# Optimization experiments

Measured on AMD Instinct MI355X. Metric: run time of the kernel, lower is better.

Reference implementation:

```python
import jax, jax.numpy as jnp
import numpy as np

N, E, DIN, HID, H, ED = 50000, 800000, 128, 64, 4, 5
Z_IDX = 3          # impedance column
PHYS_W = 1.0       # physics_weight
NEG_SLOPE = 0.2    # GATv2 leaky_relu slope


def gat_layer(x, src, dst, ea, Wl, bl, Wr, br, We, att, temp, bias, concat):
    """PhysicsGATv2Conv (add_self_loops=False, eval mode / no dropout)."""
    n = x.shape[0]
    Hh, C = att.shape
    xl = (x @ Wl + bl).reshape(n, Hh, C)   # lin_l -> source features
    xr = (x @ Wr + br).reshape(n, Hh, C)   # lin_r -> target features
    # physics-enhanced edge attr: overwrite last column with temp * w / |Z|
    z = jnp.clip(ea[:, Z_IDX], 1e-6, None)
    ea = ea.at[:, -1].set(temp * PHYS_W / z)
    e = (ea @ We).reshape(-1, Hh, C)       # lin_edge (no bias)
    m = jax.nn.leaky_relu(xl[src] + xr[dst] + e, NEG_SLOPE)  # [E,H,C]
    logit = jnp.einsum('ehc,hc->eh', m, att)                 # [E,H]
    # segment softmax over incoming edges of each target node
    lmax = jax.ops.segment_max(logit, dst, num_segments=n)
    w = jnp.exp(logit - lmax[dst])
    den = jax.ops.segment_sum(w, dst, num_segments=n)
    a = w / (den[dst] + 1e-16)
    out = jax.ops.segment_sum(xl[src] * a[:, :, None], dst, num_segments=n)
    out = out.reshape(n, Hh * C) if concat else out.mean(axis=1)
    return out + bias


def layer_norm(x, w, b):
    mu = x.mean(-1, keepdims=True)
    v = ((x - mu) ** 2).mean(-1, keepdims=True)
    return (x - mu) * jax.lax.rsqrt(v + 1e-5) * w + b


def setup_inputs() -> dict:
    key = jax.random.key(0)
    ks = iter(jax.random.split(key, 40))
    nk = lambda: next(ks)
    d = {}
    d['x'] = jax.random.normal(nk(), (N, DIN), jnp.float32)
    d['edge_index'] = jax.random.randint(nk(), (2, E), 0, N)
    d['edge_attr'] = jax.random.uniform(nk(), (E, ED), jnp.float32)
    hd = HID * H
    cfg = [(DIN, True), (hd, True), (hd, False)]
    for i, (din, concat) in enumerate(cfg):
        dout = hd if concat else HID
        d[f'Wl{i}'] = jax.random.normal(nk(), (din, hd), jnp.float32) / np.sqrt(din)
        d[f'bl{i}'] = 0.01 * jax.random.normal(nk(), (hd,), jnp.float32)
        d[f'Wr{i}'] = jax.random.normal(nk(), (din, hd), jnp.float32) / np.sqrt(din)
        d[f'br{i}'] = 0.01 * jax.random.normal(nk(), (hd,), jnp.float32)
        d[f'We{i}'] = jax.random.normal(nk(), (ED, hd), jnp.float32) / np.sqrt(ED)
        d[f'att{i}'] = jax.random.normal(nk(), (H, HID), jnp.float32) / np.sqrt(HID)
        d[f'temp{i}'] = jnp.float32(1.0)
        d[f'bias{i}'] = 0.01 * jax.random.normal(nk(), (dout,), jnp.float32)
        d[f'lnw{i}'] = jnp.ones((dout,), jnp.float32)
        d[f'lnb{i}'] = jnp.zeros((dout,), jnp.float32)
    d['pw0'] = jax.random.normal(nk(), (DIN, hd), jnp.float32) / np.sqrt(DIN)
    d['pb0'] = jnp.zeros((hd,), jnp.float32)
    d['pw2'] = jax.random.normal(nk(), (hd, HID), jnp.float32) / np.sqrt(hd)
    d['pb2'] = jnp.zeros((HID,), jnp.float32)
    return d


def reference(x, edge_index, edge_attr,
              Wl0, bl0, Wr0, br0, We0, att0, temp0, bias0, lnw0, lnb0,
              Wl1, bl1, Wr1, br1, We1, att1, temp1, bias1, lnw1, lnb1,
              Wl2, bl2, Wr2, br2, We2, att2, temp2, bias2, lnw2, lnb2,
              pw0, pb0, pw2, pb2):
    src, dst = edge_index[0], edge_index[1]
    # layer 0: 128 -> 256 (concat), residual projected
    h = gat_layer(x, src, dst, edge_attr, Wl0, bl0, Wr0, br0, We0, att0, temp0, bias0, True)
    h = layer_norm(h, lnw0, lnb0) + (x @ pw0 + pb0)
    h = jax.nn.elu(h)
    # layer 1: 256 -> 256 (concat), identity residual
    h1 = gat_layer(h, src, dst, edge_attr, Wl1, bl1, Wr1, br1, We1, att1, temp1, bias1, True)
    h = layer_norm(h1, lnw1, lnb1) + h
    h = jax.nn.elu(h)
    # layer 2: 256 -> 64 (head-mean), residual projected, no activation
    h2 = gat_layer(h, src, dst, edge_attr, Wl2, bl2, Wr2, br2, We2, att2, temp2, bias2, False)
    out = layer_norm(h2, lnw2, lnb2) + (h @ pw2 + pb2)
    return out
```

## Files before the change

kernel.cpp:

```cpp
#include <hip/hip_runtime.h>
#include <math.h>

#define NN 50000
#define EE 800000
#define NB 196

typedef _Float16 half8 __attribute__((ext_vector_type(8)));
typedef _Float16 hv4  __attribute__((ext_vector_type(4)));
typedef _Float16 hv2  __attribute__((ext_vector_type(2)));
typedef __fp16 fp16v2 __attribute__((ext_vector_type(2)));
typedef float floatx16 __attribute__((ext_vector_type(16)));
typedef float fv4 __attribute__((ext_vector_type(4)));

__device__ __forceinline__ float fexp2(float x) { return __builtin_amdgcn_exp2f(x); }

template<int CTRL>
__device__ __forceinline__ float dppadd(float x) {
    int t = __builtin_amdgcn_update_dpp(0, __float_as_int(x), CTRL, 0xf, 0xf, false);
    return x + __int_as_float(t);
}
__device__ __forceinline__ float red16(float x) {
    x = dppadd<0x121>(x);
    x = dppadd<0x122>(x);
    x = dppadd<0x124>(x);
    x = dppadd<0x128>(x);
    return x;
}

__device__ __forceinline__ unsigned int dup16(float x) {
    unsigned short b = __builtin_bit_cast(unsigned short, (_Float16)x);
    return (unsigned int)b * 0x10001u;
}
__device__ __forceinline__ unsigned int duph(float x) {
#if __has_builtin(__builtin_amdgcn_cvt_pkrtz)
    fp16v2 p = __builtin_amdgcn_cvt_pkrtz(x, x);
    return __builtin_bit_cast(unsigned int, p);
#else
    return dup16(x);
#endif
}
__device__ __forceinline__ hv4 b4(unsigned int u) {
    hv2 p = __builtin_bit_cast(hv2, u);
    return (hv4){p[0], p[1], p[0], p[1]};
}
__device__ __forceinline__ float dot4h(hv4 a, hv4 b, float c) {
    hv2 al = {a[0], a[1]}, ah = {a[2], a[3]};
    hv2 bl = {b[0], b[1]}, bh = {b[2], b[3]};
#if __has_builtin(__builtin_amdgcn_fdot2)
    return __builtin_amdgcn_fdot2(al, bl, __builtin_amdgcn_fdot2(ah, bh, c, false), false);
#else
    return c + (float)a[0]*(float)b[0] + (float)a[1]*(float)b[1]
             + (float)a[2]*(float)b[2] + (float)a[3]*(float)b[3];
#endif
}

__global__ __launch_bounds__(256) void swizzleA(
    const float* __restrict__ A, _Float16* __restrict__ Asw, int M, int K)
{
    int wave = threadIdx.x >> 6, lane = threadIdx.x & 63;
    int tile = blockIdx.x;
    int kc = blockIdx.y * 4 + wave;
    int KC = K >> 4;
    if (kc >= KC) return;
    int row = tile * 32 + (lane & 31);
    int k0 = kc * 16 + (lane >> 5) * 8;
    float4 v0 = make_float4(0.f, 0.f, 0.f, 0.f);
    float4 v1 = make_float4(0.f, 0.f, 0.f, 0.f);
    if (row < M) {
        const float* p = A + (size_t)row * K + k0;
        v0 = *(const float4*)p;
        v1 = *(const float4*)(p + 4);
    }
    half8 o;
    o[0] = (_Float16)v0.x; o[1] = (_Float16)v0.y;
    o[2] = (_Float16)v0.z; o[3] = (_Float16)v0.w;
    o[4] = (_Float16)v1.x; o[5] = (_Float16)v1.y;
    o[6] = (_Float16)v1.z; o[7] = (_Float16)v1.w;
    *(half8*)(Asw + (((size_t)tile * KC + kc) * 64 + lane) * 8) = o;
}

__global__ __launch_bounds__(256) void prep_weights(
    const float* __restrict__ s0, const float* __restrict__ s1,
    const float* __restrict__ s2, const float* __restrict__ s3,
    const float* __restrict__ s4, const float* __restrict__ s5,
    const float* __restrict__ s6, const float* __restrict__ s7,
    _Float16* __restrict__ catB0, _Float16* __restrict__ catB1,
    _Float16* __restrict__ catB2,
    const float* __restrict__ bl0, const float* __restrict__ br0,
    const float* __restrict__ pb0, const float* __restrict__ bl1,
    const float* __restrict__ br1, const float* __restrict__ bl2,
    const float* __restrict__ br2, const float* __restrict__ pb2,
    float* __restrict__ cb0, float* __restrict__ cb1, float* __restrict__ cb2,
    const float* __restrict__ We0a, const float* __restrict__ We1a,
    const float* __restrict__ We2a, const float* __restrict__ att0a,
    const float* __restrict__ att1a, const float* __restrict__ att2a,
    _Float16* __restrict__ Weh)
{
    int b = blockIdx.x;
    if (b == 192) {
        const float* Ws[3] = {We0a, We1a, We2a};
        const float* As[3] = {att0a, att1a, att2a};
        for (int t = threadIdx.x; t < 4608; t += 256) {
            int l = t / 1536, o = t - l * 1536;
            float v = (o < 1280) ? Ws[l][o] : As[l][o - 1280];
            Weh[t] = (_Float16)v;
        }
        return;
    }
    if (b >= 184) {
        int t = (b - 184) * 256 + threadIdx.x;
        if (t < 768) {
            cb0[t] = (t < 256) ? bl0[t] : (t < 512) ? br0[t - 256] : pb0[t - 512];
        } else if (t < 1280) {
            int u = t - 768;
            cb1[u] = (u < 256) ? bl1[u] : br1[u - 256];
        } else if (t < 1856) {
            int u = t - 1280;
            cb2[u] = (u < 256) ? bl2[u] : (u < 512) ? br2[u - 256] : pb2[u - 512];
        }
        return;
    }
    int wave = threadIdx.x >> 6, lane = threadIdx.x & 63;
    int pair = b * 4 + wave;
    const int cum[9] = {0, 64, 128, 192, 320, 448, 576, 704, 736};
    int job = 0;
    while (pair >= cum[job + 1]) ++job;
    const float* srcs[8] = {s0, s1, s2, s3, s4, s5, s6, s7};
    const int KCs[8] = {8, 8, 8, 16, 16, 16, 16, 16};
    const int NCs[8] = {256, 256, 256, 256, 256, 256, 256, 64};
    const int ntb[8] = {0, 8, 16, 0, 8, 0, 8, 16};
    _Float16* dsts[8] = {catB0, catB0, catB0, catB1, catB1, catB2, catB2, catB2};
    int p = pair - cum[job];
    int KC = KCs[job], NC = NCs[job];
    int nt = p / KC, kc = p - nt * KC;
    int n = (nt >> 1) * 64 + ((lane & 31) * 2) + (nt & 1);
    int k0 = kc * 16 + (lane >> 5) * 8;
    const float* B = srcs[job];
    half8 o;
#pragma unroll
    for (int jj = 0; jj < 8; ++jj)
        o[jj] = (_Float16)B[(size_t)(k0 + jj) * NC + n];
    int ntG = ntb[job] + nt;
    *(half8*)(dsts[job] + (((size_t)ntG * KC + kc) * 64 + lane) * 8) = o;
}

__global__ __launch_bounds__(256) void gemm_mfma(
    const _Float16* __restrict__ Asw, const _Float16* __restrict__ Bsw,
    const float* __restrict__ bias, _Float16* __restrict__ C,
    int M, int K, int NC)
{
    const int wave = threadIdx.x >> 6, lane = threadIdx.x & 63;
    const int KC = K >> 4;
    const int rt0 = blockIdx.x * 4 + (wave & 1) * 2;
    const int NG = NC >> 6;
    int g = blockIdx.y * 2 + (wave >> 1);
    if (g >= NG) g = NG - 1;

    const half8* Ap0 = (const half8*)Asw + (size_t)rt0 * KC * 64 + lane;
    const half8* Ap1 = Ap0 + (size_t)KC * 64;
    const half8* Bp0 = (const half8*)Bsw + (size_t)(2 * g) * KC * 64 + lane;
    const half8* Bp1 = Bp0 + (size_t)KC * 64;

    floatx16 accE0 = {0.f}, accE1 = {0.f}, accO0 = {0.f}, accO1 = {0.f};

#pragma unroll 4
    for (int kc = 0; kc < KC; ++kc) {
        half8 a0 = Ap0[(size_t)kc * 64];
        half8 a1 = Ap1[(size_t)kc * 64];
        half8 b0 = Bp0[(size_t)kc * 64];
        half8 b1 = Bp1[(size_t)kc * 64];
        accE0 = __builtin_amdgcn_mfma_f32_32x32x16_f16(a0, b0, accE0, 0, 0, 0);
        accE1 = __builtin_amdgcn_mfma_f32_32x32x16_f16(a1, b0, accE1, 0, 0, 0);
        accO0 = __builtin_amdgcn_mfma_f32_32x32x16_f16(a0, b1, accO0, 0, 0, 0);
        accO1 = __builtin_amdgcn_mfma_f32_32x32x16_f16(a1, b1, accO1, 0, 0, 0);
    }

    const int nlane = lane & 31, hs = lane >> 5;
    int colb = g * 64 + nlane * 2;
    float be = bias[colb], bo = bias[colb + 1];
#pragma unroll
    for (int r = 0; r < 16; ++r) {
        int rowin = (r & 3) + 8 * (r >> 2) + 4 * hs;
        int row0 = rt0 * 32 + rowin;
        int row1 = row0 + 32;
        if (row0 < M) {
            hv2 pe;
            pe[0] = (_Float16)(accE0[r] + be);
            pe[1] = (_Float16)(accO0[r] + bo);
            *(hv2*)(C + (size_t)row0 * NC + colb) = pe;
        }
        if (row1 < M) {
            hv2 po;
            po[0] = (_Float16)(accE1[r] + be);
            po[1] = (_Float16)(accO1[r] + bo);
            *(hv2*)(C + (size_t)row1 * NC + colb) = po;
        }
    }
}

__global__ __launch_bounds__(256) void hist_kernel(const int* __restrict__ dst,
                                                   int* __restrict__ deg)
{
    int e = blockIdx.x * 256 + threadIdx.x;
    if (e < EE) atomicAdd(&deg[dst[e]], 1);
}

__global__ __launch_bounds__(256) void scan_local(const int* __restrict__ deg,
                                                  int* __restrict__ rowoff,
                                                  int* __restrict__ part)
{
    __shared__ int sd[256];
    int tid = threadIdx.x;
    int i = blockIdx.x * 256 + tid;
    int v = (i < NN) ? deg[i] : 0;
    sd[tid] = v;
    __syncthreads();
    for (int off = 1; off < 256; off <<= 1) {
        int t = (tid >= off) ? sd[tid - off] : 0;
        __syncthreads();
        sd[tid] += t;
        __syncthreads();
    }
    if (i < NN) rowoff[i] = sd[tid] - v;
    if (tid == 255) part[blockIdx.x] = sd[255];
}

__global__ __launch_bounds__(256) void scan_part(int* __restrict__ part,
                                                 int* __restrict__ rowoff)
{
    __shared__ int sd[256];
    int tid = threadIdx.x;
    int v = (tid < NB) ? part[tid] : 0;
    sd[tid] = v;
    __syncthreads();
    for (int off = 1; off < 256; off <<= 1) {
        int t = (tid >= off) ? sd[tid - off] : 0;
        __syncthreads();
        sd[tid] += t;
        __syncthreads();
    }
    if (tid < NB) part[tid] = sd[tid] - v;
    if (tid == 0) rowoff[NN] = EE;
}

__global__ __launch_bounds__(256) void scan_add(int* __restrict__ rowoff,
                                                const int* __restrict__ part,
                                                int* __restrict__ cursor)
{
    int i = blockIdx.x * 256 + threadIdx.x;
    if (i < NN) {
        rowoff[i] += part[blockIdx.x];
        cursor[i] = 0;
    }
}

__global__ __launch_bounds__(256) void scatter_kernel(
    const int* __restrict__ src, const int* __restrict__ dst,
    const float* __restrict__ ea, const int* __restrict__ rowoff,
    int* __restrict__ cursor, int* __restrict__ srcp,
    unsigned int* __restrict__ apk, float* __restrict__ erec)
{
    int e = blockIdx.x * 256 + threadIdx.x;
    if (e < EE) {
        int d = dst[e];
        int pos = rowoff[d] + atomicAdd(&cursor[d], 1);
        srcp[pos] = src[e];
        const float* p = ea + (size_t)e * 5;
        uint4 o;
        o.x = dup16(p[0]); o.y = dup16(p[1]);
        o.z = dup16(p[2]); o.w = dup16(p[3]);
        *(uint4*)(apk + (size_t)pos * 4) = o;
        erec[pos] = 1.0f / fmaxf(p[3], 1e-6f);
    }
}

__global__ __launch_bounds__(256) void build_qtab(
    const float* __restrict__ erec, const float* __restrict__ temp,
    unsigned int* __restrict__ qtab)
{
    int e = blockIdx.x * 256 + threadIdx.x;
    if (e >= EE) return;
    float q = temp[0] * erec[e];
    float qs = fminf(q, 64.f);
    float inv = (q > 64.f) ? 64.f * __builtin_amdgcn_rcpf(q) : 1.0f;
    float sl = fmaxf(q * 0.015625f, 1.f) * 1.44269504088896340736f;
    uint4 o;
    o.x = dup16(qs);
    o.y = dup16(inv);
    o.z = __builtin_bit_cast(unsigned int, sl);
    o.w = 0u;
    *(uint4*)(qtab + (size_t)e * 4) = o;
}

template<int MODE, int RSTRIDE>
__global__ __launch_bounds__(256) void fused_attn_ln(
    const int* __restrict__ rowoff, const int* __restrict__ srcp,
    const unsigned int* __restrict__ apk, const unsigned int* __restrict__ qtab,
    const _Float16* __restrict__ xlp, const _Float16* __restrict__ Wh,
    const float* __restrict__ bias, const float* __restrict__ lnw,
    const float* __restrict__ lnb,
    const _Float16* __restrict__ residH, const float* __restrict__ residF,
    float* __restrict__ outF, _Float16* __restrict__ aswOut)
{
    int v = __builtin_amdgcn_readfirstlane(blockIdx.x * 4 + (threadIdx.x >> 6));
    int lane = threadIdx.x & 63;
    if (v >= NN) return;
    int grp = lane >> 4;
    int sub = lane & 15;
    int j = grp * 64 + sub * 4;

    hv4 ww0h = *(const hv4*)(Wh + j);
    hv4 ww1h = *(const hv4*)(Wh + 256 + j);
    hv4 ww2h = *(const hv4*)(Wh + 512 + j);
    hv4 ww3h = *(const hv4*)(Wh + 768 + j);
    hv4 ww4h = *(const hv4*)(Wh + 1024 + j);
    hv4 atvh = *(const hv4*)(Wh + 1280 + j);
    hv4 xrvh = *(const hv4*)(xlp + (size_t)v * RSTRIDE + 256 + j);
    const _Float16 s02 = (_Float16)0.2f;
    const hv4 sl02 = {s02, s02, s02, s02};
    const float L2E = 1.44269504088896340736f;

    float mxd = -INFINITY, dend = 0.f;
    fv4 acc = {0.f, 0.f, 0.f, 0.f};

    int beg = __builtin_amdgcn_readfirstlane(rowoff[v]);
    int end = __builtin_amdgcn_readfirstlane(rowoff[v + 1]);
    int i = beg;
    for (; i + 4 <= end; i += 4) {
        int s[4]; uint4 ap[4], qt[4]; hv4 xh[4]; float l[4];
#pragma unroll
        for (int u = 0; u < 4; ++u) {
            s[u] = __builtin_amdgcn_readfirstlane(srcp[i + u]);
            ap[u] = *(const uint4*)(apk + (size_t)(i + u) * 4);
            qt[u] = *(const uint4*)(qtab + (size_t)(i + u) * 4);
        }
#pragma unroll
        for (int u = 0; u < 4; ++u)
            xh[u] = *(const hv4*)(xlp + (size_t)s[u] * RSTRIDE + j);
#pragma unroll
        for (int u = 0; u < 4; ++u) {
            hv4 t = xh[u] + xrvh;
            t += b4(ap[u].x) * ww0h;
            t += b4(ap[u].y) * ww1h;
            t += b4(ap[u].z) * ww2h;
            t += b4(ap[u].w) * ww3h;
            hv4 m = b4(qt[u].x) * ww4h;
            m += b4(qt[u].y) * t;
            hv4 mn = m * sl02;
            m = __builtin_elementwise_max(m, mn);
            l[u] = dot4h(m, atvh, 0.f);
        }
#pragma unroll
        for (int u = 0; u < 4; ++u)
            l[u] = red16(l[u]) * __builtin_bit_cast(float, qt[u].z);
        float nm = fmaxf(fmaxf(l[0], l[1]), fmaxf(l[2], l[3]));
        nm = fmaxf(nm, mxd);
        float sc = fexp2(mxd - nm);
        float e0 = fexp2(l[0] - nm);
        float e1 = fexp2(l[1] - nm);
        float e2 = fexp2(l[2] - nm);
        float e3 = fexp2(l[3] - nm);
        mxd = nm;
        dend = dend * sc + ((e0 + e1) + (e2 + e3));
        hv4 X = xh[0] * b4(duph(e0));
        X += xh[1] * b4(duph(e1));
        X += xh[2] * b4(duph(e2));
        X += xh[3] * b4(duph(e3));
        fv4 Xf = __builtin_convertvector(X, fv4);
        acc = acc * sc + Xf;
    }
    for (; i < end; ++i) {
        int s0 = __builtin_amdgcn_readfirstlane(srcp[i]);
        uint4 ap = *(const uint4*)(apk + (size_t)i * 4);
        uint4 qt = *(const uint4*)(qtab + (size_t)i * 4);
        hv4 xh = *(const hv4*)(xlp + (size_t)s0 * RSTRIDE + j);
        hv4 t = xh + xrvh;
        t += b4(ap.x) * ww0h;
        t += b4(ap.y) * ww1h;
        t += b4(ap.z) * ww2h;
        t += b4(ap.w) * ww3h;
        hv4 m = b4(qt.x) * ww4h;
        m += b4(qt.y) * t;
        hv4 mn = m * sl02;
        m = __builtin_elementwise_max(m, mn);
        float l0 = dot4h(m, atvh, 0.f);
        l0 = red16(l0) * __builtin_bit_cast(float, qt.z);
        float nm = fmaxf(mxd, l0);
        float sc = fexp2(mxd - nm);
        float e0 = fexp2(l0 - nm);
        mxd = nm;
        dend = dend * sc + e0;
        fv4 xf = __builtin_convertvector(xh, fv4);
        acc = acc * sc + xf * e0;
    }

    float inv = __builtin_amdgcn_rcpf(dend + 1e-16f);
    if (MODE <= 1) {
        fv4 bb = *(const fv4*)(bias + j);
        fv4 o = acc * inv + bb;
        float s  = (o[0] + o[1]) + (o[2] + o[3]);
        fv4 oq = o * o;
        float s2 = (oq[0] + oq[1]) + (oq[2] + oq[3]);
        s = red16(s);   s += __shfl_xor(s, 16, 64);  s += __shfl_xor(s, 32, 64);
        s2 = red16(s2); s2 += __shfl_xor(s2, 16, 64); s2 += __shfl_xor(s2, 32, 64);
        float mu = s * (1.f / 256.f);
        float var = s2 * (1.f / 256.f) - mu * mu;
        float rs = __builtin_amdgcn_rsqf(var + 1e-5f);
        fv4 lw = *(const fv4*)(lnw + j);
        fv4 lb = *(const fv4*)(lnb + j);
        fv4 rr;
        if (MODE == 0)
            rr = __builtin_convertvector(
                *(const hv4*)(residH + (size_t)v * RSTRIDE + j), fv4);
        else
            rr = *(const fv4*)(residF + (size_t)v * 256 + j);
        fv4 y = (o - mu) * rs * lw + lb + rr;
        y[0] = (y[0] > 0.f) ? y[0] : fexp2(y[0] * L2E) - 1.f;
        y[1] = (y[1] > 0.f) ? y[1] : fexp2(y[1] * L2E) - 1.f;
        y[2] = (y[2] > 0.f) ? y[2] : fexp2(y[2] * L2E) - 1.f;
        y[3] = (y[3] > 0.f) ? y[3] : fexp2(y[3] * L2E) - 1.f;
        if (MODE == 0)
            *(fv4*)(outF + (size_t)v * 256 + j) = y;
        int kc = j >> 4, half = (j >> 3) & 1, off = j & 7;
        size_t idx = (((size_t)(v >> 5) * 16 + kc) * 64 + (v & 31) + 32 * half) * 8 + off;
        hv4 yh = __builtin_convertvector(y, hv4);
        *(hv4*)(aswOut + idx) = yh;
    } else {
        fv4 r = acc * inv;
        r[0] += __shfl_xor(r[0], 16, 64); r[0] += __shfl_xor(r[0], 32, 64);
        r[1] += __shfl_xor(r[1], 16, 64); r[1] += __shfl_xor(r[1], 32, 64);
        r[2] += __shfl_xor(r[2], 16, 64); r[2] += __shfl_xor(r[2], 32, 64);
        r[3] += __shfl_xor(r[3], 16, 64); r[3] += __shfl_xor(r[3], 32, 64);
        fv4 bb = *(const fv4*)(bias + sub * 4);
        fv4 o = r * 0.25f + bb;
        float s  = (o[0] + o[1]) + (o[2] + o[3]);
        fv4 oq = o * o;
        float s2 = (oq[0] + oq[1]) + (oq[2] + oq[3]);
        s = red16(s);
        s2 = red16(s2);
        float mu = s * (1.f / 64.f);
        float var = s2 * (1.f / 64.f) - mu * mu;
        float rs = __builtin_amdgcn_rsqf(var + 1e-5f);
        fv4 lw = *(const fv4*)(lnw + sub * 4);
        fv4 lb = *(const fv4*)(lnb + sub * 4);
        fv4 rr = __builtin_convertvector(
            *(const hv4*)(residH + (size_t)v * RSTRIDE + sub * 4), fv4);
        fv4 y = (o - mu) * rs * lw + lb + rr;
        if (grp == 0)
            *(fv4*)(outF + (size_t)v * 64 + sub * 4) = y;
    }
}

extern "C" void kernel_launch(void* const* d_in, const int* in_sizes, int n_in,
                              void* d_out, int out_size, void* d_ws, size_t ws_size,
                              hipStream_t stream)
{
    const float* x    = (const float*)d_in[0];
    const int*   eidx = (const int*)d_in[1];
    const float* ea   = (const float*)d_in[2];
    const int* src = eidx;
    const int* dst = eidx + EE;

    const float *Wl[3], *bl[3], *Wr[3], *br[3], *We[3], *att[3], *temp[3],
                *bias[3], *lnw[3], *lnb[3];
    for (int i = 0; i < 3; ++i) {
        int b = 3 + i * 10;
        Wl[i]   = (const float*)d_in[b + 0];
        bl[i]   = (const float*)d_in[b + 1];
        Wr[i]   = (const float*)d_in[b + 2];
        br[i]   = (const float*)d_in[b + 3];
        We[i]   = (const float*)d_in[b + 4];
        att[i]  = (const float*)d_in[b + 5];
        temp[i] = (const float*)d_in[b + 6];
        bias[i] = (const float*)d_in[b + 7];
        lnw[i]  = (const float*)d_in[b + 8];
        lnb[i]  = (const float*)d_in[b + 9];
    }
    const float* pw0 = (const float*)d_in[33];
    const float* pb0 = (const float*)d_in[34];
    const float* pw2 = (const float*)d_in[35];
    const float* pb2 = (const float*)d_in[36];

    char* w = (char*)d_ws;
    float* h     = (float*)w; w += (size_t)NN * 256 * 4;
    char*  gbase = w;         w += (size_t)NN * 256 * 4;
    _Float16* xlr = (_Float16*)w; w += (size_t)NN * 768 * 2;
    unsigned int* apk = (unsigned int*)w; w += (size_t)EE * 16;
    float* erec  = (float*)w; w += (size_t)EE * 4;
    int* srcp    = (int*)w;   w += (size_t)EE * 4;
    int* rowoff  = (int*)w;   w += (size_t)(NN + 16) * 4;
    int* cursor  = (int*)w;   w += (size_t)NN * 4;
    int* part    = (int*)w;   w += 1024;
    w = (char*)(((uintptr_t)w + 255) & ~(uintptr_t)255);
    _Float16* catB0 = (_Float16*)w; w += 196608;
    _Float16* catB1 = (_Float16*)w; w += 262144;
    _Float16* catB2 = (_Float16*)w; w += 294912;
    float* cb0 = (float*)w; w += 768 * 4;
    float* cb1 = (float*)w; w += 512 * 4;
    float* cb2 = (float*)w; w += 576 * 4;
    _Float16* Weh = (_Float16*)w; w += 4608 * 2;
    _Float16* Asw = (_Float16*)gbase;
    unsigned int* qtab = (unsigned int*)(gbase + 38400000);

    dim3 blk(256);
    dim3 grid_e((EE + 255) / 256);
    dim3 grid_nw((NN + 3) / 4);
    dim3 grid_nb(NB);
    const int MT = 391;

    hipMemsetAsync(cursor, 0, (size_t)NN * 4, stream);
    hipLaunchKernelGGL(hist_kernel, grid_e, blk, 0, stream, dst, cursor);
    hipLaunchKernelGGL(scan_local, grid_nb, blk, 0, stream, cursor, rowoff, part);
    hipLaunchKernelGGL(scan_part, dim3(1), blk, 0, stream, part, rowoff);
    hipLaunchKernelGGL(scan_add, grid_nb, blk, 0, stream, rowoff, part, cursor);
    hipLaunchKernelGGL(scatter_kernel, grid_e, blk, 0, stream,
                       src, dst, ea, rowoff, cursor, srcp, apk, erec);

    hipLaunchKernelGGL(prep_weights, dim3(193), blk, 0, stream,
                       Wl[0], Wr[0], pw0, Wl[1], Wr[1], Wl[2], Wr[2], pw2,
                       catB0, catB1, catB2,
                       bl[0], br[0], pb0, bl[1], br[1], bl[2], br[2], pb2,
                       cb0, cb1, cb2,
                       We[0], We[1], We[2], att[0], att[1], att[2], Weh);

    swizzleA<<<dim3(1564, 2), blk, 0, stream>>>(x, Asw, NN, 128);
    hipLaunchKernelGGL(build_qtab, grid_e, blk, 0, stream, erec, temp[0], qtab);
    gemm_mfma<<<dim3(MT, 6), blk, 0, stream>>>(
        Asw, catB0, cb0, xlr, NN, 128, 768);
    fused_attn_ln<0, 768><<<grid_nw, blk, 0, stream>>>(
        rowoff, srcp, apk, qtab, xlr, Weh,
        bias[0], lnw[0], lnb[0], xlr + 512, nullptr, h, Asw);

    hipLaunchKernelGGL(build_qtab, grid_e, blk, 0, stream, erec, temp[1], qtab);
    gemm_mfma<<<dim3(MT, 4), blk, 0, stream>>>(
        Asw, catB1, cb1, xlr, NN, 256, 512);
    fused_attn_ln<1, 512><<<grid_nw, blk, 0, stream>>>(
        rowoff, srcp, apk, qtab, xlr, Weh + 1536,
        bias[1], lnw[1], lnb[1], nullptr, h, h, Asw);

    hipLaunchKernelGGL(build_qtab, grid_e, blk, 0, stream, erec, temp[2], qtab);
    gemm_mfma<<<dim3(MT, 5), blk, 0, stream>>>(
        Asw, catB2, cb2, xlr, NN, 256, 576);
    fused_attn_ln<2, 576><<<grid_nw, blk, 0, stream>>>(
        rowoff, srcp, apk, qtab, xlr, Weh + 3072,
        bias[2], lnw[2], lnb[2], xlr + 512, nullptr, (float*)d_out, nullptr);
}
```

Before: 641.3 us.

## Unroll edge loop to 8 with dual softmax accumulators and lazy rescale

The per-node edge aggregation loop now processes 8 edges per iteration. It issues all 8 gathered source-row loads up front to raise memory-level parallelism, and splits the work into two independent online-softmax accumulator chains that are merged after the loop. Rescaling of the running max is skipped unless some lane sees a new maximum, which avoids exp and multiply work in the common case. In exchange the kernel uses more registers, which may lower occupancy, and it adds wave-wide vote branches.

```diff
diff --git a/kernel.cpp b/kernel.cpp
--- a/kernel.cpp
+++ b/kernel.cpp
@@ -322,58 +322,10 @@
 
     float mxd = -INFINITY, dend = 0.f;
     fv4 acc = {0.f, 0.f, 0.f, 0.f};
-
-    int beg = __builtin_amdgcn_readfirstlane(rowoff[v]);
-    int end = __builtin_amdgcn_readfirstlane(rowoff[v + 1]);
-    int i = beg;
-    for (; i + 4 <= end; i += 4) {
-        int s[4]; uint4 ap[4], qt[4]; hv4 xh[4]; float l[4];
-#pragma unroll
-        for (int u = 0; u < 4; ++u) {
-            s[u] = __builtin_amdgcn_readfirstlane(srcp[i + u]);
-            ap[u] = *(const uint4*)(apk + (size_t)(i + u) * 4);
-            qt[u] = *(const uint4*)(qtab + (size_t)(i + u) * 4);
-        }
-#pragma unroll
-        for (int u = 0; u < 4; ++u)
-            xh[u] = *(const hv4*)(xlp + (size_t)s[u] * RSTRIDE + j);
-#pragma unroll
-        for (int u = 0; u < 4; ++u) {
-            hv4 t = xh[u] + xrvh;
-            t += b4(ap[u].x) * ww0h;
-            t += b4(ap[u].y) * ww1h;
-            t += b4(ap[u].z) * ww2h;
-            t += b4(ap[u].w) * ww3h;
-            hv4 m = b4(qt[u].x) * ww4h;
-            m += b4(qt[u].y) * t;
-            hv4 mn = m * sl02;
-            m = __builtin_elementwise_max(m, mn);
-            l[u] = dot4h(m, atvh, 0.f);
-        }
-#pragma unroll
-        for (int u = 0; u < 4; ++u)
-            l[u] = red16(l[u]) * __builtin_bit_cast(float, qt[u].z);
-        float nm = fmaxf(fmaxf(l[0], l[1]), fmaxf(l[2], l[3]));
-        nm = fmaxf(nm, mxd);
-        float sc = fexp2(mxd - nm);
-        float e0 = fexp2(l[0] - nm);
-        float e1 = fexp2(l[1] - nm);
-        float e2 = fexp2(l[2] - nm);
-        float e3 = fexp2(l[3] - nm);
-        mxd = nm;
-        dend = dend * sc + ((e0 + e1) + (e2 + e3));
-        hv4 X = xh[0] * b4(duph(e0));
-        X += xh[1] * b4(duph(e1));
-        X += xh[2] * b4(duph(e2));
-        X += xh[3] * b4(duph(e3));
-        fv4 Xf = __builtin_convertvector(X, fv4);
-        acc = acc * sc + Xf;
-    }
-    for (; i < end; ++i) {
-        int s0 = __builtin_amdgcn_readfirstlane(srcp[i]);
-        uint4 ap = *(const uint4*)(apk + (size_t)i * 4);
-        uint4 qt = *(const uint4*)(qtab + (size_t)i * 4);
-        hv4 xh = *(const hv4*)(xlp + (size_t)s0 * RSTRIDE + j);
+    float mxB = -INFINITY, denB = 0.f;
+    fv4 accB = {0.f, 0.f, 0.f, 0.f};
+
+    auto SCORE = [&](hv4 xh, uint4 ap, uint4 qt) -> float {
         hv4 t = xh + xrvh;
         t += b4(ap.x) * ww0h;
         t += b4(ap.y) * ww1h;
@@ -383,15 +335,106 @@
         m += b4(qt.y) * t;
         hv4 mn = m * sl02;
         m = __builtin_elementwise_max(m, mn);
-        float l0 = dot4h(m, atvh, 0.f);
-        l0 = red16(l0) * __builtin_bit_cast(float, qt.z);
-        float nm = fmaxf(mxd, l0);
-        float sc = fexp2(mxd - nm);
-        float e0 = fexp2(l0 - nm);
+        float l = dot4h(m, atvh, 0.f);
+        return red16(l) * __builtin_bit_cast(float, qt.z);
+    };
+    auto GRP = [&](float& MX, float& DD, fv4& AC,
+                   float la, float lb, float lc, float ld,
+                   hv4 xa, hv4 xb, hv4 xc, hv4 xd) {
+        float nm = fmaxf(fmaxf(la, lb), fmaxf(lc, ld));
+        if (__any(nm > MX)) {
+            nm = fmaxf(nm, MX);
+            float sc = fexp2(MX - nm);
+            MX = nm;
+            DD *= sc;
+            AC *= sc;
+        }
+        float e0 = fexp2(la - MX), e1 = fexp2(lb - MX);
+        float e2 = fexp2(lc - MX), e3 = fexp2(ld - MX);
+        DD += (e0 + e1) + (e2 + e3);
+        hv4 X = xa * b4(duph(e0));
+        X += xb * b4(duph(e1));
+        X += xc * b4(duph(e2));
+        X += xd * b4(duph(e3));
+        AC += __builtin_convertvector(X, fv4);
+    };
+
+    int beg = __builtin_amdgcn_readfirstlane(rowoff[v]);
+    int end = __builtin_amdgcn_readfirstlane(rowoff[v + 1]);
+    int i = beg;
+    for (; i + 8 <= end; i += 8) {
+        int s[8];
+#pragma unroll
+        for (int u = 0; u < 8; ++u)
+            s[u] = __builtin_amdgcn_readfirstlane(srcp[i + u]);
+        hv4 xh[8];
+#pragma unroll
+        for (int u = 0; u < 8; ++u)
+            xh[u] = *(const hv4*)(xlp + (size_t)s[u] * RSTRIDE + j);
+        uint4 apA[4], qtA[4];
+#pragma unroll
+        for (int u = 0; u < 4; ++u) {
+            apA[u] = *(const uint4*)(apk + (size_t)(i + u) * 4);
+            qtA[u] = *(const uint4*)(qtab + (size_t)(i + u) * 4);
+        }
+        float l0 = SCORE(xh[0], apA[0], qtA[0]);
+        float l1 = SCORE(xh[1], apA[1], qtA[1]);
+        float l2 = SCORE(xh[2], apA[2], qtA[2]);
+        float l3 = SCORE(xh[3], apA[3], qtA[3]);
+        GRP(mxd, dend, acc, l0, l1, l2, l3, xh[0], xh[1], xh[2], xh[3]);
+        uint4 apB[4], qtB[4];
+#pragma unroll
+        for (int u = 0; u < 4; ++u) {
+            apB[u] = *(const uint4*)(apk + (size_t)(i + 4 + u) * 4);
+            qtB[u] = *(const uint4*)(qtab + (size_t)(i + 4 + u) * 4);
+        }
+        float l4 = SCORE(xh[4], apB[0], qtB[0]);
+        float l5 = SCORE(xh[5], apB[1], qtB[1]);
+        float l6 = SCORE(xh[6], apB[2], qtB[2]);
+        float l7 = SCORE(xh[7], apB[3], qtB[3]);
+        GRP(mxB, denB, accB, l4, l5, l6, l7, xh[4], xh[5], xh[6], xh[7]);
+    }
+    if (i != beg) {
+        float nm = fmaxf(mxd, mxB);
+        float sA = fexp2(mxd - nm), sB = fexp2(mxB - nm);
+        dend = dend * sA + denB * sB;
+        acc = acc * sA + accB * sB;
         mxd = nm;
-        dend = dend * sc + e0;
+    }
+    for (; i + 4 <= end; i += 4) {
+        int s[4]; uint4 ap[4], qt[4]; hv4 xh[4];
+#pragma unroll
+        for (int u = 0; u < 4; ++u) {
+            s[u] = __builtin_amdgcn_readfirstlane(srcp[i + u]);
+            ap[u] = *(const uint4*)(apk + (size_t)(i + u) * 4);
+            qt[u] = *(const uint4*)(qtab + (size_t)(i + u) * 4);
+        }
+#pragma unroll
+        for (int u = 0; u < 4; ++u)
+            xh[u] = *(const hv4*)(xlp + (size_t)s[u] * RSTRIDE + j);
+        float l0 = SCORE(xh[0], ap[0], qt[0]);
+        float l1 = SCORE(xh[1], ap[1], qt[1]);
+        float l2 = SCORE(xh[2], ap[2], qt[2]);
+        float l3 = SCORE(xh[3], ap[3], qt[3]);
+        GRP(mxd, dend, acc, l0, l1, l2, l3, xh[0], xh[1], xh[2], xh[3]);
+    }
+    for (; i < end; ++i) {
+        int s0 = __builtin_amdgcn_readfirstlane(srcp[i]);
+        uint4 ap = *(const uint4*)(apk + (size_t)i * 4);
+        uint4 qt = *(const uint4*)(qtab + (size_t)i * 4);
+        hv4 xh = *(const hv4*)(xlp + (size_t)s0 * RSTRIDE + j);
+        float l0 = SCORE(xh, ap, qt);
+        if (__any(l0 > mxd)) {
+            float nm = fmaxf(l0, mxd);
+            float sc = fexp2(mxd - nm);
+            mxd = nm;
+            dend *= sc;
+            acc *= sc;
+        }
+        float e0 = fexp2(l0 - mxd);
+        dend += e0;
         fv4 xf = __builtin_convertvector(xh, fv4);
-        acc = acc * sc + xf * e0;
+        acc += xf * e0;
     }
 
     float inv = __builtin_amdgcn_rcpf(dend + 1e-16f);
```

Measured after the change: 645.4 us. About the same (+0.6%).
